# Kernel tuning notes

Hardware: AMD Instinct MI355X
Metric: run time of the kernel (lower is better)

Reference implementation:

```python
import jax, jax.numpy as jnp
import numpy as np

B = 262144
NUM_FEA = 32
EMB_DIM = 8
OUT_DIM = 16

def setup_inputs() -> dict:
    key = jax.random.key(0)
    ks = jax.random.split(key, 6)
    x = jax.random.normal(ks[0], (B, NUM_FEA), dtype=jnp.float32)
    # per-feature Dense(1 -> emb_dim): weight row + bias per feature
    emb_W = jax.random.normal(ks[1], (NUM_FEA, EMB_DIM), dtype=jnp.float32) * 0.5
    emb_b = jax.random.normal(ks[2], (NUM_FEA, EMB_DIM), dtype=jnp.float32) * 0.1
    M = jax.random.normal(ks[3], (EMB_DIM, EMB_DIM), dtype=jnp.float32) * (1.0 / np.sqrt(EMB_DIM))
    dense_W = jax.random.normal(ks[4], (NUM_FEA, OUT_DIM), dtype=jnp.float32) * (1.0 / np.sqrt(NUM_FEA))
    dense_b = jax.random.normal(ks[5], (OUT_DIM,), dtype=jnp.float32) * 0.1
    return {"x": x, "emb_W": emb_W, "emb_b": emb_b, "M": M,
            "dense_W": dense_W, "dense_b": dense_b}

def reference(x, emb_W, emb_b, M, dense_W, dense_b):
    mid = x.shape[1] // 2  # 16
    # fused batched per-feature Dense(1 -> emb_dim): [B, F, E]
    emb = x[:, :, None] * emb_W[None, :, :] + emb_b[None, :, :]
    left = emb[:, :mid, :]    # [B, mid, E]
    right = emb[:, mid:, :]   # [B, mid, E]
    # bilinear co-attention: G = tanh(left @ M @ right^T), [B, mid, mid]
    G = jnp.tanh(jnp.einsum('ble,ef,brf->blr', left, M, right))
    lr = jax.nn.softmax(G.sum(axis=1), axis=-1)  # [B, mid]
    rl = jax.nn.softmax(G.sum(axis=2), axis=-1)  # [B, mid]
    a = jnp.concatenate([lr, rl], axis=-1)       # [B, F]
    out = x * a
    # mix == 'concat': Dense(16, relu)
    return jax.nn.relu(out @ dense_W + dense_b)
```

## Files before the change

kernel.cpp:

```cpp
#include <hip/hip_runtime.h>
#include <hip/hip_bf16.h>


#if __has_builtin(__builtin_amdgcn_exp2f)
#define EXP2F(v) __builtin_amdgcn_exp2f(v)
#else
#define EXP2F(v) exp2f(v)
#endif

#if __has_builtin(__builtin_amdgcn_rcpf)
#define RCPF(v) __builtin_amdgcn_rcpf(v)
#else
#define RCPF(v) (1.0f / (v))
#endif

#define LOG2E 1.4426950408889634f

__device__ __forceinline__ float fast_tanh(float v) {
    float E = EXP2F(v * (2.0f * LOG2E));
    return 1.0f - 2.0f * RCPF(E + 1.0f);
}

__global__ __launch_bounds__(256) void coattn_kernel(
    const float* __restrict__ x,
    const float* __restrict__ emb_W,
    const float* __restrict__ emb_b,
    const float* __restrict__ M,
    const float* __restrict__ dW,
    const float* __restrict__ db,
    float* __restrict__ out)
{
    const int i = blockIdx.x * blockDim.x + threadIdx.x;

    float xv[32];
    const float4* xp = reinterpret_cast<const float4*>(x + (size_t)i * 32);
    #pragma unroll
    for (int k = 0; k < 8; ++k) {
        float4 v = xp[k];
        xv[4*k+0] = v.x; xv[4*k+1] = v.y; xv[4*k+2] = v.z; xv[4*k+3] = v.w;
    }

    float MR[16][8];
    #pragma unroll
    for (int r = 0; r < 16; ++r) {
        float re[8];
        #pragma unroll
        for (int f = 0; f < 8; ++f)
            re[f] = fmaf(xv[16 + r], emb_W[(16 + r) * 8 + f], emb_b[(16 + r) * 8 + f]);
        #pragma unroll
        for (int e = 0; e < 8; ++e) {
            float acc = M[e * 8 + 0] * re[0];
            #pragma unroll
            for (int f = 1; f < 8; ++f)
                acc = fmaf(M[e * 8 + f], re[f], acc);
            MR[r][e] = acc;
        }
    }

    float colsum[16], rowsum[16];
    #pragma unroll
    for (int r = 0; r < 16; ++r) colsum[r] = 0.0f;

    #pragma unroll
    for (int l = 0; l < 16; ++l) {
        float le[8];
        #pragma unroll
        for (int e = 0; e < 8; ++e)
            le[e] = fmaf(xv[l], emb_W[l * 8 + e], emb_b[l * 8 + e]);
        float rs = 0.0f;
        #pragma unroll
        for (int r = 0; r < 16; ++r) {
            float g = le[0] * MR[r][0];
            #pragma unroll
            for (int e = 1; e < 8; ++e)
                g = fmaf(le[e], MR[r][e], g);
            float t = fast_tanh(g);
            rs += t;
            colsum[r] += t;
        }
        rowsum[l] = rs;
    }

    float a[32];
    {
        float s = 0.0f;
        #pragma unroll
        for (int r = 0; r < 16; ++r) {
            float e = EXP2F(colsum[r] * LOG2E);
            a[r] = e; s += e;
        }
        float inv = RCPF(s);
        #pragma unroll
        for (int r = 0; r < 16; ++r) a[r] *= inv;
    }
    {
        float s = 0.0f;
        #pragma unroll
        for (int l = 0; l < 16; ++l) {
            float e = EXP2F(rowsum[l] * LOG2E);
            a[16 + l] = e; s += e;
        }
        float inv = RCPF(s);
        #pragma unroll
        for (int l = 0; l < 16; ++l) a[16 + l] *= inv;
    }

    float o[16];
    #pragma unroll
    for (int k = 0; k < 16; ++k) o[k] = db[k];
    #pragma unroll
    for (int j = 0; j < 32; ++j) {
        float v = xv[j] * a[j];
        #pragma unroll
        for (int k = 0; k < 16; ++k)
            o[k] = fmaf(v, dW[j * 16 + k], o[k]);
    }

    float4* op = reinterpret_cast<float4*>(out + (size_t)i * 16);
    #pragma unroll
    for (int k = 0; k < 4; ++k) {
        float4 v;
        v.x = fmaxf(o[4*k+0], 0.0f);
        v.y = fmaxf(o[4*k+1], 0.0f);
        v.z = fmaxf(o[4*k+2], 0.0f);
        v.w = fmaxf(o[4*k+3], 0.0f);
        op[k] = v;
    }
}

extern "C" void kernel_launch(void* const* d_in, const int* in_sizes, int n_in,
                              void* d_out, int out_size, void* d_ws, size_t ws_size,
                              hipStream_t stream) {
    const float* x     = (const float*)d_in[0];
    const float* emb_W = (const float*)d_in[1];
    const float* emb_b = (const float*)d_in[2];
    const float* M     = (const float*)d_in[3];
    const float* dW    = (const float*)d_in[4];
    const float* db    = (const float*)d_in[5];
    float* out = (float*)d_out;

    const int B = in_sizes[0] / 32;
    dim3 block(256);
    dim3 grid((B + 255) / 256);
    hipLaunchKernelGGL(coattn_kernel, grid, block, 0, stream,
                       x, emb_W, emb_b, M, dW, db, out);
}
```

Before: 126.0 us.

## Precompute bilinear coefficients so each logit is two FMAs per pair

```diff
diff --git a/kernel.cpp b/kernel.cpp
--- a/kernel.cpp
+++ b/kernel.cpp
@@ -16,16 +16,48 @@
 
 #define LOG2E 1.4426950408889634f
 
-__device__ __forceinline__ float fast_tanh(float v) {
-    float E = EXP2F(v * (2.0f * LOG2E));
-    return 1.0f - 2.0f * RCPF(E + 1.0f);
+__global__ __launch_bounds__(256) void coattn_setup(
+    const float* __restrict__ emb_W,
+    const float* __restrict__ emb_b,
+    const float* __restrict__ M,
+    float* __restrict__ C)
+{
+    const int t = threadIdx.x;
+    const int l = t >> 4;
+    const int r = t & 15;
+
+    float MW[8], Mb[8];
+    #pragma unroll
+    for (int e = 0; e < 8; ++e) {
+        float s1 = 0.0f, s2 = 0.0f;
+        #pragma unroll
+        for (int f = 0; f < 8; ++f) {
+            float m = M[e * 8 + f];
+            s1 = fmaf(m, emb_W[(16 + r) * 8 + f], s1);
+            s2 = fmaf(m, emb_b[(16 + r) * 8 + f], s2);
+        }
+        MW[e] = s1; Mb[e] = s2;
+    }
+    float c1 = 0.0f, c2 = 0.0f, c3 = 0.0f, c4 = 0.0f;
+    #pragma unroll
+    for (int e = 0; e < 8; ++e) {
+        float w = emb_W[l * 8 + e];
+        float b = emb_b[l * 8 + e];
+        c1 = fmaf(w, MW[e], c1);
+        c2 = fmaf(w, Mb[e], c2);
+        c3 = fmaf(b, MW[e], c3);
+        c4 = fmaf(b, Mb[e], c4);
+    }
+    const float s = 2.0f * LOG2E;
+    C[0 * 256 + l * 16 + r] = c1 * s;
+    C[1 * 256 + l * 16 + r] = c2 * s;
+    C[2 * 256 + l * 16 + r] = c3 * s;
+    C[3 * 256 + l * 16 + r] = c4 * s;
 }
 
 __global__ __launch_bounds__(256) void coattn_kernel(
     const float* __restrict__ x,
-    const float* __restrict__ emb_W,
-    const float* __restrict__ emb_b,
-    const float* __restrict__ M,
+    const float* __restrict__ C,
     const float* __restrict__ dW,
     const float* __restrict__ db,
     float* __restrict__ out)
@@ -40,43 +72,24 @@
         xv[4*k+0] = v.x; xv[4*k+1] = v.y; xv[4*k+2] = v.z; xv[4*k+3] = v.w;
     }
 
-    float MR[16][8];
+    float colsum[16];
     #pragma unroll
-    for (int r = 0; r < 16; ++r) {
-        float re[8];
-        #pragma unroll
-        for (int f = 0; f < 8; ++f)
-            re[f] = fmaf(xv[16 + r], emb_W[(16 + r) * 8 + f], emb_b[(16 + r) * 8 + f]);
-        #pragma unroll
-        for (int e = 0; e < 8; ++e) {
-            float acc = M[e * 8 + 0] * re[0];
-            #pragma unroll
-            for (int f = 1; f < 8; ++f)
-                acc = fmaf(M[e * 8 + f], re[f], acc);
-            MR[r][e] = acc;
-        }
-    }
-
-    float colsum[16], rowsum[16];
-    #pragma unroll
-    for (int r = 0; r < 16; ++r) colsum[r] = 0.0f;
+    for (int r = 0; r < 16; ++r) colsum[r] = 16.0f;
+    float rowsum[16];
 
     #pragma unroll
     for (int l = 0; l < 16; ++l) {
-        float le[8];
-        #pragma unroll
-        for (int e = 0; e < 8; ++e)
-            le[e] = fmaf(xv[l], emb_W[l * 8 + e], emb_b[l * 8 + e]);
-        float rs = 0.0f;
+        const float xl = xv[l];
+        float rs = 16.0f;
         #pragma unroll
         for (int r = 0; r < 16; ++r) {
-            float g = le[0] * MR[r][0];
-            #pragma unroll
-            for (int e = 1; e < 8; ++e)
-                g = fmaf(le[e], MR[r][e], g);
-            float t = fast_tanh(g);
-            rs += t;
-            colsum[r] += t;
+            const float xr = xv[16 + r];
+            float u  = xr * C[0 * 256 + l * 16 + r] + C[1 * 256 + l * 16 + r];
+            float v2 = xr * C[2 * 256 + l * 16 + r] + C[3 * 256 + l * 16 + r];
+            float g  = fmaf(xl, u, v2);
+            float rc = RCPF(EXP2F(g) + 1.0f);
+            rs         = fmaf(-2.0f, rc, rs);
+            colsum[r]  = fmaf(-2.0f, rc, colsum[r]);
         }
         rowsum[l] = rs;
     }
@@ -138,10 +151,14 @@
     const float* dW    = (const float*)d_in[4];
     const float* db    = (const float*)d_in[5];
     float* out = (float*)d_out;
+    float* C   = (float*)d_ws;
+
+    hipLaunchKernelGGL(coattn_setup, dim3(1), dim3(256), 0, stream,
+                       emb_W, emb_b, M, C);
 
     const int B = in_sizes[0] / 32;
     dim3 block(256);
     dim3 grid((B + 255) / 256);
     hipLaunchKernelGGL(coattn_kernel, grid, block, 0, stream,
-                       x, emb_W, emb_b, M, dW, db, out);
+                       x, C, dW, db, out);
 }
```

Measured after the change: 110.8 us. 1.14x faster.
